# Performance work log

Measured on AMD Instinct MI355X. Metric: run time of the kernel, lower is better.

The kernel has to match this reference:

```python
import jax, jax.numpy as jnp
import numpy as np

H = 64  # hidden_size
B, S, DIN = 256, 4096, 1
NUM_LAYERS = 3


def setup_inputs() -> dict:
    key = jax.random.key(0)
    ks = jax.random.split(key, 32)
    s = 1.0 / np.sqrt(H)  # torch LSTM/Linear init bound
    inp = {"x": jax.random.normal(ks[0], (B, S, DIN), dtype=jnp.float32)}
    ki = 1
    for l in range(NUM_LAYERS):
        din = DIN if l == 0 else H
        inp[f"Wih{l}"] = jax.random.uniform(ks[ki], (4 * H, din), minval=-s, maxval=s); ki += 1
        inp[f"Whh{l}"] = jax.random.uniform(ks[ki], (4 * H, H), minval=-s, maxval=s); ki += 1
        inp[f"bih{l}"] = jax.random.uniform(ks[ki], (4 * H,), minval=-s, maxval=s); ki += 1
        inp[f"bhh{l}"] = jax.random.uniform(ks[ki], (4 * H,), minval=-s, maxval=s); ki += 1
    inp["Wlin"] = jax.random.uniform(ks[ki], (1, H), minval=-s, maxval=s); ki += 1
    inp["blin"] = jax.random.uniform(ks[ki], (1,), minval=-s, maxval=s)
    return inp


def _lstm_layer(x, Wih, Whh, bih, bhh):
    """x: [B,S,Din] -> (hs [B,S,H], h_T [B,H], c_T [B,H]). PyTorch gate order i,f,g,o."""
    # precompute input contribution for all timesteps (one big GEMM)
    xg = jnp.einsum('bsd,gd->bsg', x, Wih) + (bih + bhh)  # [B,S,4H]
    b = x.shape[0]
    h0 = jnp.zeros((b, H), x.dtype)
    c0 = jnp.zeros((b, H), x.dtype)

    def step(carry, xg_t):
        h, c = carry
        g = xg_t + h @ Whh.T  # [B,4H]
        i, f, gg, o = jnp.split(g, 4, axis=-1)
        c = jax.nn.sigmoid(f) * c + jax.nn.sigmoid(i) * jnp.tanh(gg)
        h = jax.nn.sigmoid(o) * jnp.tanh(c)
        return (h, c), h

    (hT, cT), hs = jax.lax.scan(step, (h0, c0), jnp.swapaxes(xg, 0, 1))
    return jnp.swapaxes(hs, 0, 1), hT, cT


def reference(x, Wih0, Whh0, bih0, bhh0, Wih1, Whh1, bih1, bhh1,
              Wih2, Whh2, bih2, bhh2, Wlin, blin):
    layers = [(Wih0, Whh0, bih0, bhh0), (Wih1, Whh1, bih1, bhh1), (Wih2, Whh2, bih2, bhh2)]
    out = x
    hTs, cTs = [], []
    for (Wih, Whh, bih, bhh) in layers:
        out, hT, cT = _lstm_layer(out, Wih, Whh, bih, bhh)
        hTs.append(hT); cTs.append(cT)
    y = out @ Wlin.T + blin  # [B,S,1]
    h_n = jnp.stack(hTs, axis=0)  # [num_layers,B,H]
    c_n = jnp.stack(cTs, axis=0)
    return y, h_n, c_n
```

## Files before the change

kernel.cpp:

```cpp
#include <hip/hip_runtime.h>
#include <stdint.h>


#define SQ 4096
#define HH 64
#define NB 256

typedef _Float16 h2    __attribute__((ext_vector_type(2)));
typedef _Float16 f16x8 __attribute__((ext_vector_type(8)));
typedef float    f32x4 __attribute__((ext_vector_type(4)));

template<int CTRL>
__device__ __forceinline__ float fdpp(float v) {
    return __builtin_bit_cast(float,
        __builtin_amdgcn_mov_dpp(__builtin_bit_cast(int, v), CTRL, 0xF, 0xF, true));
}
#define DPP_XOR1 0xB1
#define DPP_XOR2 0x4E
#define DPP_ROR4 0x124
#define DPP_ROR8 0x128

__device__ __forceinline__ float frcp(float x)  { return __builtin_amdgcn_rcpf(x); }
__device__ __forceinline__ float fexp2(float x) { return __builtin_amdgcn_exp2f(x); }

__device__ __forceinline__ void pin4(uint4& r) {
    asm volatile("" : "+v"(r.x), "+v"(r.y), "+v"(r.z), "+v"(r.w));
}
__device__ __forceinline__ void pinf(float& x) { asm volatile("" : "+v"(x)); }

__device__ __forceinline__ f32x4 mm(uint4 hv, uint4 wv, f32x4 c) {
    return __builtin_amdgcn_mfma_f32_16x16x32_f16(
        __builtin_bit_cast(f16x8, hv), __builtin_bit_cast(f16x8, wv), c, 0, 0, 0);
}

__global__ __launch_bounds__(256)
void prep_weights(const float* __restrict__ Whh0, const float* __restrict__ Wih1,
                  const float* __restrict__ Whh1, const float* __restrict__ Wih2,
                  const float* __restrict__ Whh2, uint32_t* __restrict__ ws)
{
    const int idx = blockIdx.x * 256 + threadIdx.x;
    int r, ktbits;
    const float *Wi = nullptr, *Wh;
    if (idx < 8192)       { r = idx;         ktbits = 1; Wh = Whh0; }
    else if (idx < 24576) { r = idx - 8192;  ktbits = 2; Wi = Wih1; Wh = Whh1; }
    else                  { r = idx - 24576; ktbits = 2; Wi = Wih2; Wh = Whh2; }
    const int jj  = r & 3;
    const int l   = (r >> 2) & 63;
    const int rem = r >> 8;
    const int kt  = rem & ((1 << ktbits) - 1);
    const int tw  = rem >> ktbits;
    const int j   = tw & 3;
    const int w   = tw >> 2;
    const int n   = l & 15;
    const int krow = ((l >> 4) << 3) + 2 * jj;
    const int orow = 64 * j + 16 * w + n;
    int kcol = 32 * kt + krow;
    const float* M;
    if (ktbits == 1)    { M = Wh; }
    else if (kcol < 64) { M = Wi; }
    else                { M = Wh; kcol -= 64; }
    h2 t;
    t[0] = (_Float16)M[orow * HH + kcol];
    t[1] = (_Float16)M[orow * HH + kcol + 1];
    ws[idx] = __builtin_bit_cast(uint32_t, t);
}

__global__ __launch_bounds__(768)
__attribute__((amdgpu_waves_per_eu(1, 3)))
void lstm3_fused(
    const float* __restrict__ x,
    const float* __restrict__ Wih0,
    const float* __restrict__ bih0, const float* __restrict__ bhh0,
    const float* __restrict__ bih1, const float* __restrict__ bhh1,
    const float* __restrict__ bih2, const float* __restrict__ bhh2,
    const float* __restrict__ Wlin, const float* __restrict__ blin,
    const uint32_t* __restrict__ wpk,
    float* __restrict__ out)
{
    const int b    = blockIdx.x;
    const int tid  = threadIdx.x;
    const int grp  = tid >> 8;
    const int k    = tid & 255;
    const int w    = k >> 6;
    const int l    = k & 63;
    const int n    = l & 15;
    const int q    = l >> 4;
    const bool act16 = (l < 16);
    const int unit = 16 * w + n;

    __shared__ __align__(16) float xrow[SQ];
    __shared__ __align__(16) uint4 hbf[2][3][8];
    __shared__ __align__(16) float ybuf[2][4];

    for (int i = tid; i < SQ; i += 768) xrow[i] = x[b * SQ + i];
    if (tid < 48) ((uint4*)hbf)[tid] = make_uint4(0, 0, 0, 0);
    if (tid < 8) ((float*)ybuf)[tid] = 0.f;

    const int gbase = (grp == 0) ? 0 : (grp == 1) ? 8192 : 24576;
    const int KT    = (grp == 0) ? 2 : 4;
    const uint32_t* wbp = wpk + gbase;
    auto fr = [&](int j_, int kt_) {
        return *reinterpret_cast<const uint4*>(
            wbp + (((w * 4 + j_) * KT + kt_) * 64 + l) * 4);
    };
    uint4 w00 = fr(0, 0), w01 = fr(0, 1), w10 = fr(1, 0), w11 = fr(1, 1),
          w20 = fr(2, 0), w21 = fr(2, 1), w30 = fr(3, 0), w31 = fr(3, 1);
    pin4(w00); pin4(w01); pin4(w10); pin4(w11);
    pin4(w20); pin4(w21); pin4(w30); pin4(w31);
    uint4 w02 = {}, w03 = {}, w12 = {}, w13 = {},
          w22 = {}, w23 = {}, w32 = {}, w33 = {};
    if (grp != 0) {
        w02 = fr(0, 2); w03 = fr(0, 3); w12 = fr(1, 2); w13 = fr(1, 3);
        w22 = fr(2, 2); w23 = fr(2, 3); w32 = fr(3, 2); w33 = fr(3, 3);
        pin4(w02); pin4(w03); pin4(w12); pin4(w13);
        pin4(w22); pin4(w23); pin4(w32); pin4(w33);
    }

    const float* bi = (grp == 0) ? bih0 : (grp == 1) ? bih1 : bih2;
    const float* bh = (grp == 0) ? bhh0 : (grp == 1) ? bhh1 : bhh2;
    float bs0 = bi[unit]       + bh[unit];
    float bs1 = bi[64 + unit]  + bh[64 + unit];
    float bs2 = bi[128 + unit] + bh[128 + unit];
    float bs3 = bi[192 + unit] + bh[192 + unit];
    pinf(bs0); pinf(bs1); pinf(bs2); pinf(bs3);
    float wx0 = 0.f, wx1 = 0.f, wx2 = 0.f, wx3 = 0.f, wl = 0.f;
    if (grp == 0) {
        wx0 = Wih0[unit];       wx1 = Wih0[64 + unit];
        wx2 = Wih0[128 + unit]; wx3 = Wih0[192 + unit];
        pinf(wx0); pinf(wx1); pinf(wx2); pinf(wx3);
    } else if (grp == 2) {
        wl = Wlin[unit]; pinf(wl);
    }
    const float blin_v = blin[0];

    const int la = (grp == 2) ? 1 : 0;
    const int lb = grp;
    const uint4* pA[2] = { &hbf[0][la][q], &hbf[1][la][q] };
    const uint4* pB[2] = { &hbf[0][lb][q], &hbf[1][lb][q] };
    _Float16* pH[2] = { (_Float16*)&hbf[0][grp][0] + unit,
                        (_Float16*)&hbf[1][grp][0] + unit };

    const f32x4 Z = {0.f, 0.f, 0.f, 0.f};
    float cc = 0.f;

    __syncthreads();

    auto tick = [&](int T, int rd) {
        const int wr = rd ^ 1;

        const uint4 a0 = pA[rd][0], a1 = pA[rd][4];
        f32x4 d0 = mm(a0, w00, Z);  f32x4 d1 = mm(a0, w10, Z);
        f32x4 d2 = mm(a0, w20, Z);  f32x4 d3 = mm(a0, w30, Z);
        d0 = mm(a1, w01, d0);  d1 = mm(a1, w11, d1);
        d2 = mm(a1, w21, d2);  d3 = mm(a1, w31, d3);
        if (grp != 0) {
            const uint4 c0 = pB[rd][0], c1 = pB[rd][4];
            d0 = mm(c0, w02, d0);  d1 = mm(c0, w12, d1);
            d2 = mm(c0, w22, d2);  d3 = mm(c0, w32, d3);
            d0 = mm(c1, w03, d0);  d1 = mm(c1, w13, d1);
            d2 = mm(c1, w23, d2);  d3 = mm(c1, w33, d3);
        }

        const int step = T - grp;
        float yv = 0.f;
        if (act16 && step >= 0 && step < SQ) {
            float gi = d0[0] + bs0;
            float gf = d1[0] + bs1;
            float gg = d2[0] + bs2;
            float go = d3[0] + bs3;
            if (grp == 0) {
                const float xT = xrow[T];
                gi += wx0 * xT; gf += wx1 * xT;
                gg += wx2 * xT; go += wx3 * xT;
            }
            const float i_ = frcp(1.f + fexp2(gi * -1.44269504f));
            const float f_ = frcp(1.f + fexp2(gf * -1.44269504f));
            const float o_ = frcp(1.f + fexp2(go * -1.44269504f));
            const float tg = 2.f * frcp(1.f + fexp2(gg * -2.88539008f)) - 1.f;
            cc = f_ * cc + i_ * tg;
            const float tc = fminf(fmaxf(cc, -15.f), 15.f);
            const float e  = fexp2(tc * -2.88539008f);
            const float h  = o_ * ((1.f - e) * frcp(1.f + e));
            pH[wr][0] = (_Float16)h;
            if (grp == 2) yv = wl * h;
            if (step == SQ - 1) {
                out[NB * SQ + grp * NB * HH + b * HH + unit] = h;
                out[NB * SQ + 3 * NB * HH + grp * NB * HH + b * HH + unit] = cc;
            }
        }
        if (grp == 2) {
            yv += fdpp<DPP_XOR1>(yv);
            yv += fdpp<DPP_XOR2>(yv);
            yv += fdpp<DPP_ROR4>(yv);
            yv += fdpp<DPP_ROR8>(yv);
            if (l == 0) ybuf[rd][w] = yv;
        }
        if (grp == 0 && w == 3 && l == 16) {
            const int sy = T - 3;
            if (sy >= 0 && sy < SQ) {
                const float4 v = *(const float4*)ybuf[rd ^ 1];
                out[b * SQ + sy] = (v.x + v.y) + (v.z + v.w) + blin_v;
            }
        }
        __syncthreads();
    };

    for (int T = 0; T < SQ + 4; T += 2) {
        tick(T, 0);
        tick(T + 1, 1);
    }
}

extern "C" void kernel_launch(void* const* d_in, const int* in_sizes, int n_in,
                              void* d_out, int out_size, void* d_ws, size_t ws_size,
                              hipStream_t stream) {
    const float* x    = (const float*)d_in[0];
    const float* Wih0 = (const float*)d_in[1];
    const float* Whh0 = (const float*)d_in[2];
    const float* bih0 = (const float*)d_in[3];
    const float* bhh0 = (const float*)d_in[4];
    const float* Wih1 = (const float*)d_in[5];
    const float* Whh1 = (const float*)d_in[6];
    const float* bih1 = (const float*)d_in[7];
    const float* bhh1 = (const float*)d_in[8];
    const float* Wih2 = (const float*)d_in[9];
    const float* Whh2 = (const float*)d_in[10];
    const float* bih2 = (const float*)d_in[11];
    const float* bhh2 = (const float*)d_in[12];
    const float* Wlin = (const float*)d_in[13];
    const float* blin = (const float*)d_in[14];
    float* out = (float*)d_out;

    uint32_t* wpk = (uint32_t*)d_ws;
    prep_weights<<<160, 256, 0, stream>>>(Whh0, Wih1, Whh1, Wih2, Whh2, wpk);
    lstm3_fused<<<NB, 768, 0, stream>>>(x, Wih0, bih0, bhh0,
                                        bih1, bhh1, bih2, bhh2,
                                        Wlin, blin, wpk, out);
}
```

Before: 2.830 ms.

## Compute output projection via MFMA and fold gate biases into accumulators

The final linear projection is computed with two extra MFMAs on layer-2 wave 0. Each reads the layer-2 hidden state already staged in shared memory, against a packed Wlin fragment produced by the prep kernel. This replaces the per-tick DPP reduction, the ybuf shared-memory round trip and the extra store path on group 0. Gate biases are pre-broadcast into the MFMA accumulator inputs, so the scalar bias adds disappear. The activation math now runs on all lanes, with only stores masked. This trades the act16 branch for redundant work and adds two MFMAs to one wave's per-step critical path.

```diff
diff --git a/kernel.cpp b/kernel.cpp
--- a/kernel.cpp
+++ b/kernel.cpp
@@ -10,23 +10,17 @@
 typedef _Float16 f16x8 __attribute__((ext_vector_type(8)));
 typedef float    f32x4 __attribute__((ext_vector_type(4)));
 
-template<int CTRL>
-__device__ __forceinline__ float fdpp(float v) {
-    return __builtin_bit_cast(float,
-        __builtin_amdgcn_mov_dpp(__builtin_bit_cast(int, v), CTRL, 0xF, 0xF, true));
-}
-#define DPP_XOR1 0xB1
-#define DPP_XOR2 0x4E
-#define DPP_ROR4 0x124
-#define DPP_ROR8 0x128
-
 __device__ __forceinline__ float frcp(float x)  { return __builtin_amdgcn_rcpf(x); }
 __device__ __forceinline__ float fexp2(float x) { return __builtin_amdgcn_exp2f(x); }
 
 __device__ __forceinline__ void pin4(uint4& r) {
     asm volatile("" : "+v"(r.x), "+v"(r.y), "+v"(r.z), "+v"(r.w));
 }
-__device__ __forceinline__ void pinf(float& x) { asm volatile("" : "+v"(x)); }
+__device__ __forceinline__ void pinv(f32x4& r) {
+    float t0 = r[0], t1 = r[1], t2 = r[2], t3 = r[3];
+    asm volatile("" : "+v"(t0), "+v"(t1), "+v"(t2), "+v"(t3));
+    r[0] = t0; r[1] = t1; r[2] = t2; r[3] = t3;
+}
 
 __device__ __forceinline__ f32x4 mm(uint4 hv, uint4 wv, f32x4 c) {
     return __builtin_amdgcn_mfma_f32_16x16x32_f16(
@@ -36,9 +30,24 @@
 __global__ __launch_bounds__(256)
 void prep_weights(const float* __restrict__ Whh0, const float* __restrict__ Wih1,
                   const float* __restrict__ Whh1, const float* __restrict__ Wih2,
-                  const float* __restrict__ Whh2, uint32_t* __restrict__ ws)
+                  const float* __restrict__ Whh2, const float* __restrict__ Wlin,
+                  uint32_t* __restrict__ ws)
 {
     const int idx = blockIdx.x * 256 + threadIdx.x;
+    if (idx >= 40960) {
+        const int r  = idx - 40960;
+        const int jj = r & 3;
+        const int l  = (r >> 2) & 63;
+        const int kk = (r >> 8) & 1;
+        const int n  = l & 15;
+        const int krow = ((l >> 4) << 3) + 2 * jj;
+        const int ku   = 32 * kk + krow;
+        h2 t;
+        t[0] = (_Float16)((n == 0) ? Wlin[ku]     : 0.f);
+        t[1] = (_Float16)((n == 0) ? Wlin[ku + 1] : 0.f);
+        ws[idx] = __builtin_bit_cast(uint32_t, t);
+        return;
+    }
     int r, ktbits;
     const float *Wi = nullptr, *Wh;
     if (idx < 8192)       { r = idx;         ktbits = 1; Wh = Whh0; }
@@ -73,7 +82,7 @@
     const float* __restrict__ bih0, const float* __restrict__ bhh0,
     const float* __restrict__ bih1, const float* __restrict__ bhh1,
     const float* __restrict__ bih2, const float* __restrict__ bhh2,
-    const float* __restrict__ Wlin, const float* __restrict__ blin,
+    const float* __restrict__ blin,
     const uint32_t* __restrict__ wpk,
     float* __restrict__ out)
 {
@@ -85,16 +94,14 @@
     const int l    = k & 63;
     const int n    = l & 15;
     const int q    = l >> 4;
-    const bool act16 = (l < 16);
     const int unit = 16 * w + n;
+    const bool grp2w0 = (grp == 2) && (w == 0);
 
     __shared__ __align__(16) float xrow[SQ];
     __shared__ __align__(16) uint4 hbf[2][3][8];
-    __shared__ __align__(16) float ybuf[2][4];
 
     for (int i = tid; i < SQ; i += 768) xrow[i] = x[b * SQ + i];
     if (tid < 48) ((uint4*)hbf)[tid] = make_uint4(0, 0, 0, 0);
-    if (tid < 8) ((float*)ybuf)[tid] = 0.f;
 
     const int gbase = (grp == 0) ? 0 : (grp == 1) ? 8192 : 24576;
     const int KT    = (grp == 0) ? 2 : 4;
@@ -115,23 +122,33 @@
         pin4(w02); pin4(w03); pin4(w12); pin4(w13);
         pin4(w22); pin4(w23); pin4(w32); pin4(w33);
     }
+    uint4 wy2 = {}, wy3 = {};
+    f32x4 cy = {0.f, 0.f, 0.f, 0.f};
+    if (grp2w0) {
+        wy2 = *reinterpret_cast<const uint4*>(wpk + 40960 + (0 * 64 + l) * 4);
+        wy3 = *reinterpret_cast<const uint4*>(wpk + 40960 + (1 * 64 + l) * 4);
+        pin4(wy2); pin4(wy3);
+        const float bv = blin[0];
+        cy = f32x4{bv, bv, bv, bv};
+        pinv(cy);
+    }
 
     const float* bi = (grp == 0) ? bih0 : (grp == 1) ? bih1 : bih2;
     const float* bh = (grp == 0) ? bhh0 : (grp == 1) ? bhh1 : bhh2;
-    float bs0 = bi[unit]       + bh[unit];
-    float bs1 = bi[64 + unit]  + bh[64 + unit];
-    float bs2 = bi[128 + unit] + bh[128 + unit];
-    float bs3 = bi[192 + unit] + bh[192 + unit];
-    pinf(bs0); pinf(bs1); pinf(bs2); pinf(bs3);
-    float wx0 = 0.f, wx1 = 0.f, wx2 = 0.f, wx3 = 0.f, wl = 0.f;
+    const float bs0 = bi[unit]       + bh[unit];
+    const float bs1 = bi[64 + unit]  + bh[64 + unit];
+    const float bs2 = bi[128 + unit] + bh[128 + unit];
+    const float bs3 = bi[192 + unit] + bh[192 + unit];
+    f32x4 cb0 = {bs0, bs0, bs0, bs0};  pinv(cb0);
+    f32x4 cb1 = {bs1, bs1, bs1, bs1};  pinv(cb1);
+    f32x4 cb2 = {bs2, bs2, bs2, bs2};  pinv(cb2);
+    f32x4 cb3 = {bs3, bs3, bs3, bs3};  pinv(cb3);
+
+    float wx0 = 0.f, wx1 = 0.f, wx2 = 0.f, wx3 = 0.f;
     if (grp == 0) {
         wx0 = Wih0[unit];       wx1 = Wih0[64 + unit];
         wx2 = Wih0[128 + unit]; wx3 = Wih0[192 + unit];
-        pinf(wx0); pinf(wx1); pinf(wx2); pinf(wx3);
-    } else if (grp == 2) {
-        wl = Wlin[unit]; pinf(wl);
-    }
-    const float blin_v = blin[0];
+    }
 
     const int la = (grp == 2) ? 1 : 0;
     const int lb = grp;
@@ -140,17 +157,20 @@
     _Float16* pH[2] = { (_Float16*)&hbf[0][grp][0] + unit,
                         (_Float16*)&hbf[1][grp][0] + unit };
 
-    const f32x4 Z = {0.f, 0.f, 0.f, 0.f};
     float cc = 0.f;
 
     __syncthreads();
 
     auto tick = [&](int T, int rd) {
         const int wr = rd ^ 1;
+        float xT = 0.f;
+        if (grp == 0) xT = xrow[(T < SQ) ? T : 0];
 
         const uint4 a0 = pA[rd][0], a1 = pA[rd][4];
-        f32x4 d0 = mm(a0, w00, Z);  f32x4 d1 = mm(a0, w10, Z);
-        f32x4 d2 = mm(a0, w20, Z);  f32x4 d3 = mm(a0, w30, Z);
+        f32x4 d0 = mm(a0, w00, cb0);
+        f32x4 d1 = mm(a0, w10, cb1);
+        f32x4 d2 = mm(a0, w20, cb2);
+        f32x4 d3 = mm(a0, w30, cb3);
         d0 = mm(a1, w01, d0);  d1 = mm(a1, w11, d1);
         d2 = mm(a1, w21, d2);  d3 = mm(a1, w31, d3);
         if (grp != 0) {
@@ -159,17 +179,19 @@
             d2 = mm(c0, w22, d2);  d3 = mm(c0, w32, d3);
             d0 = mm(c1, w03, d0);  d1 = mm(c1, w13, d1);
             d2 = mm(c1, w23, d2);  d3 = mm(c1, w33, d3);
+            if (grp2w0) {
+                f32x4 d4 = mm(c0, wy2, cy);
+                d4 = mm(c1, wy3, d4);
+                const int sy = T - 3;
+                if (l == 0 && sy >= 0 && sy < SQ)
+                    out[b * SQ + sy] = d4[0];
+            }
         }
 
         const int step = T - grp;
-        float yv = 0.f;
-        if (act16 && step >= 0 && step < SQ) {
-            float gi = d0[0] + bs0;
-            float gf = d1[0] + bs1;
-            float gg = d2[0] + bs2;
-            float go = d3[0] + bs3;
+        if (step >= 0 && step < SQ) {
+            float gi = d0[0], gf = d1[0], gg = d2[0], go = d3[0];
             if (grp == 0) {
-                const float xT = xrow[T];
                 gi += wx0 * xT; gf += wx1 * xT;
                 gg += wx2 * xT; go += wx3 * xT;
             }
@@ -181,25 +203,12 @@
             const float tc = fminf(fmaxf(cc, -15.f), 15.f);
             const float e  = fexp2(tc * -2.88539008f);
             const float h  = o_ * ((1.f - e) * frcp(1.f + e));
-            pH[wr][0] = (_Float16)h;
-            if (grp == 2) yv = wl * h;
-            if (step == SQ - 1) {
-                out[NB * SQ + grp * NB * HH + b * HH + unit] = h;
-                out[NB * SQ + 3 * NB * HH + grp * NB * HH + b * HH + unit] = cc;
-            }
-        }
-        if (grp == 2) {
-            yv += fdpp<DPP_XOR1>(yv);
-            yv += fdpp<DPP_XOR2>(yv);
-            yv += fdpp<DPP_ROR4>(yv);
-            yv += fdpp<DPP_ROR8>(yv);
-            if (l == 0) ybuf[rd][w] = yv;
-        }
-        if (grp == 0 && w == 3 && l == 16) {
-            const int sy = T - 3;
-            if (sy >= 0 && sy < SQ) {
-                const float4 v = *(const float4*)ybuf[rd ^ 1];
-                out[b * SQ + sy] = (v.x + v.y) + (v.z + v.w) + blin_v;
+            if (l < 16) {
+                pH[wr][0] = (_Float16)h;
+                if (step == SQ - 1) {
+                    out[NB * SQ + grp * NB * HH + b * HH + unit] = h;
+                    out[NB * SQ + 3 * NB * HH + grp * NB * HH + b * HH + unit] = cc;
+                }
             }
         }
         __syncthreads();
@@ -232,8 +241,8 @@
     float* out = (float*)d_out;
 
     uint32_t* wpk = (uint32_t*)d_ws;
-    prep_weights<<<160, 256, 0, stream>>>(Whh0, Wih1, Whh1, Wih2, Whh2, wpk);
+    prep_weights<<<162, 256, 0, stream>>>(Whh0, Wih1, Whh1, Wih2, Whh2, Wlin, wpk);
     lstm3_fused<<<NB, 768, 0, stream>>>(x, Wih0, bih0, bhh0,
                                         bih1, bhh1, bih2, bhh2,
-                                        Wlin, blin, wpk, out);
-}
+                                        blin, wpk, out);
+}
```

Measured after the change: 2.616 ms. 7.6% less time.
